# Performance work log

Hardware: AMD Instinct MI355X
Metric: run time of the kernel (lower is better)

## Reference

```python
import jax, jax.numpy as jnp
import numpy as np

B, S, N, D, NAMED, NTYPES = 8, 64, 100, 1024, 768, 5

def _ln(x, g, b, eps=1e-5):
    m = x.mean(-1, keepdims=True)
    v = ((x - m) ** 2).mean(-1, keepdims=True)
    return (x - m) * jax.lax.rsqrt(v + eps) * g + b

def _lin(x, W, b=None):
    y = x @ W.T
    return y if b is None else y + b

def setup_inputs():
    key = jax.random.key(0)
    ks = jax.random.split(key, 24)
    p = lambda i, shape, s=0.02: jax.random.normal(ks[i], shape, jnp.float32) * s
    inp = {}
    inp['scene_reps'] = jax.random.normal(ks[0], (B, S, D), jnp.float32)
    u = jax.random.uniform(ks[1], (B, N, S))
    keep = (jax.random.uniform(ks[2], (B, N, S)) < 0.25).astype(jnp.float32)
    inp['incidence_matrix'] = u * keep
    inp['edge_type_ids'] = jax.random.randint(ks[3], (B, S), 0, NTYPES)
    inp['entity_type_ids'] = jax.random.randint(ks[4], (B, N), 0, NTYPES)
    inp['entity_mask'] = jax.random.uniform(ks[5], (B, N)) < 0.9
    inp['entity_name_embs'] = jax.random.normal(ks[6], (B, N, NAMED), jnp.float32)
    inp['type_embed'] = p(7, (NTYPES, D), 1.0)
    inp['name_W'] = p(8, (D, NAMED))
    inp['name_ln_g'] = jnp.ones(D); inp['name_ln_b'] = jnp.zeros(D)
    inp['n2e_W'] = p(9, (D, D)); inp['n2e_b'] = jnp.zeros(D)
    inp['t2e_W'] = p(10, (D, D)); inp['t2e_b'] = jnp.zeros(D)
    inp['edge_ln_g'] = jnp.ones(D); inp['edge_ln_b'] = jnp.zeros(D)
    inp['gate_W1'] = p(11, (D // 4, D)); inp['gate_b1'] = jnp.zeros(D // 4)
    inp['gate_W2'] = p(12, (3, D // 4)); inp['gate_b2'] = jnp.zeros(3)
    inp['ms_W'] = p(13, (D, D)); inp['ms_b'] = jnp.zeros(D)
    inp['ma_W'] = p(14, (D, D)); inp['ma_b'] = jnp.zeros(D)
    inp['mi_W'] = p(15, (D, D)); inp['mi_b'] = jnp.zeros(D)
    inp['role_w'] = p(16, (D,))
    inp['gru_Wih'] = p(17, (3 * D, D)); inp['gru_Whh'] = p(18, (3 * D, D))
    inp['gru_bih'] = jnp.zeros(3 * D); inp['gru_bhh'] = jnp.zeros(3 * D)
    inp['upd_ln_g'] = jnp.ones(D); inp['upd_ln_b'] = jnp.zeros(D)
    inp['eo_W'] = p(19, (D, D)); inp['eo_b'] = jnp.zeros(D)
    inp['eo_ln_g'] = jnp.ones(D); inp['eo_ln_b'] = jnp.zeros(D)
    inp['res_ln_g'] = jnp.ones(D); inp['res_ln_b'] = jnp.zeros(D)
    return inp

def reference(scene_reps, incidence_matrix, edge_type_ids, entity_type_ids, entity_mask, entity_name_embs, type_embed, name_W, name_ln_g, name_ln_b, n2e_W, n2e_b, t2e_W, t2e_b, edge_ln_g, edge_ln_b, gate_W1, gate_b1, gate_W2, gate_b2, ms_W, ms_b, ma_W, ma_b, mi_W, mi_b, role_w, gru_Wih, gru_Whh, gru_bih, gru_bhh, upd_ln_g, upd_ln_b, eo_W, eo_b, eo_ln_g, eo_ln_b, res_ln_g, res_ln_b):
    # edge_type_ids is accepted by the torch module but unused in its forward.
    dt = scene_reps.dtype
    emaskf = entity_mask.astype(dt)  # [B,N]
    h0 = type_embed[entity_type_ids] + _ln(_lin(entity_name_embs, name_W), name_ln_g, name_ln_b)
    h0 = h0 * emaskf[..., None]
    eye = jnp.eye(N, dtype=dt)
    step_ids = jnp.arange(S)

    def step(carry, xs):
        h, ebuf = carry  # h [B,N,D], ebuf [B,S,D] (hyperedge history)
        s, x_s, inc_s = xs  # x_s [B,D], inc_s [B,N]
        roles = inc_s * emaskf
        wsum = jnp.maximum(roles.sum(1, keepdims=True), 1.0)
        mean_ent = jnp.einsum('bn,bnd->bd', roles, h) / wsum
        e_s = _ln(_lin(mean_ent, n2e_W, n2e_b) + _lin(x_s, t2e_W, t2e_b), edge_ln_g, edge_ln_b)
        in_mask = (roles > 0).astype(dt)[..., None]  # [B,N,1]
        msg_scene = _lin(e_s, ms_W, ms_b)[:, None, :]
        # arc stream: attention over past hyperedges with exponential recency decay
        valid = (step_ids < s).astype(dt)
        denom = jnp.maximum(s - 1, 1).astype(dt)
        decay = jnp.exp(-1.0 + step_ids.astype(dt) / denom) * valid  # linspace(-1,0,s)
        arc = incidence_matrix * roles[:, :, None] * decay[None, None, :]  # [B,N,S]
        arc = arc / jnp.maximum(arc.sum(-1, keepdims=True), 1e-8)
        msg_arc = _lin(jnp.einsum('bns,bsd->bnd', arc, jax.lax.stop_gradient(ebuf)), ma_W, ma_b)
        msg_arc = jnp.where(s > 0, msg_arc, jnp.zeros_like(msg_arc))
        # interaction stream: entity co-occurrence within the scene
        co = roles[:, :, None] * roles[:, None, :] * (1.0 - eye)
        co = co / jnp.maximum(co.sum(-1, keepdims=True), 1e-8)
        msg_int = _lin(jnp.einsum('bnm,bmd->bnd', co, h), mi_W, mi_b)
        gate = jax.nn.softmax(_lin(jax.nn.gelu(_lin(e_s, gate_W1, gate_b1), approximate=False), gate_W2, gate_b2), axis=-1)  # [B,3]
        msg = gate[:, 0, None, None] * msg_scene + gate[:, 1, None, None] * msg_arc + gate[:, 2, None, None] * msg_int
        msg = msg + (roles[..., None] * role_w) * in_mask
        # GRUCell (torch semantics) + LayerNorm, masked update
        gi = _lin(msg, gru_Wih, gru_bih)
        gh = _lin(h, gru_Whh, gru_bhh)
        i_r, i_z, i_n = jnp.split(gi, 3, axis=-1)
        h_r, h_z, h_n = jnp.split(gh, 3, axis=-1)
        r = jax.nn.sigmoid(i_r + h_r)
        z = jax.nn.sigmoid(i_z + h_z)
        n = jnp.tanh(i_n + r * h_n)
        h_new = jnp.clip(_ln((1 - z) * n + z * h, upd_ln_g, upd_ln_b), -50.0, 50.0)
        h = h * (1 - in_mask) + h_new * in_mask
        ebuf = ebuf.at[:, s].set(e_s)
        return (h, ebuf), e_s

    ebuf0 = jnp.zeros((B, S, D), dt)
    (h_fin, _), es = jax.lax.scan(step, (h0, ebuf0), (step_ids, scene_reps.transpose(1, 0, 2), incidence_matrix.transpose(2, 0, 1)))
    H = es.transpose(1, 0, 2)  # [B,S,D]
    H = _ln(H + scene_reps, res_ln_g, res_ln_b)
    H = _ln(jax.nn.gelu(_lin(H, eo_W, eo_b), approximate=False), eo_ln_g, eo_ln_b)
    return (H, h_fin)
```

## Files before the change

kernel.cpp:

```cpp
#include <hip/hip_runtime.h>
#include <math.h>

#define B_   8
#define S_   64
#define N_   100
#define D_   1024
#define ND_  768
#define BN_  800
#define G3_  3072
#define G6_  6144
#define HC7  7168
#define RSC  0.00390625f

typedef _Float16 f16x8 __attribute__((ext_vector_type(8)));
typedef float f32x4 __attribute__((ext_vector_type(4)));

#define MFMA16(a,b,c) __builtin_amdgcn_mfma_f32_16x16x32_f16(a, b, c, 0, 0, 0)

static __device__ __forceinline__ float wave_sum(float v) {
    for (int off = 32; off > 0; off >>= 1) v += __shfl_down(v, off, 64);
    return v;
}

static __device__ __forceinline__ float wave_allsum(float v) {
    for (int off = 1; off < 64; off <<= 1) v += __shfl_xor(v, off, 64);
    return v;
}

static __device__ __forceinline__ float block_sum(float v) {
    __shared__ float red_[8];
    float w = wave_sum(v);
    int lane = threadIdx.x & 63, wid = threadIdx.x >> 6;
    __syncthreads();
    if (lane == 0) red_[wid] = w;
    __syncthreads();
    float t = 0.f;
    for (int i = 0; i < 4; ++i) t += red_[i];
    return t;
}

static __device__ __forceinline__ float gelu_f(float x) {
    return 0.5f * x * (1.f + erff(x * 0.70710678118654752f));
}

static __device__ __forceinline__ unsigned short f2h(float x) {
    union { _Float16 h; unsigned short u; } c; c.h = (_Float16)x; return c.u;
}

__global__ __launch_bounds__(256) void k_f2h(
    const float* __restrict__ src, unsigned short* __restrict__ dst,
    int rows, int cols, int ldd)
{
    size_t n = (size_t)rows * cols;
    size_t i = ((size_t)blockIdx.x * 256 + threadIdx.x) * 4;
    if (i >= n) return;
    int r = (int)(i / cols);
    int c = (int)(i - (size_t)r * cols);
    float4 v = *(const float4*)(src + i);
    ushort4 o; o.x = f2h(v.x); o.y = f2h(v.y); o.z = f2h(v.z); o.w = f2h(v.w);
    *(ushort4*)(dst + (size_t)r * ldd + c) = o;
}

__global__ __launch_bounds__(256) void k_f2hT(
    const float* __restrict__ src, unsigned short* __restrict__ dst,
    int R, int C, int ldd, int rowoff)
{
    __shared__ _Float16 T[32][33];
    int tr = threadIdx.x >> 3, tc4 = (threadIdx.x & 7) * 4;
    int r0 = blockIdx.y * 32, c0 = blockIdx.x * 32;
    float4 v = *(const float4*)(src + (size_t)(r0 + tr) * C + c0 + tc4);
    T[tc4][tr] = (_Float16)v.x; T[tc4+1][tr] = (_Float16)v.y;
    T[tc4+2][tr] = (_Float16)v.z; T[tc4+3][tr] = (_Float16)v.w;
    __syncthreads();
    union { _Float16 h; unsigned short u; } cv;
    ushort4 o;
    cv.h = T[tr][tc4];   o.x = cv.u;
    cv.h = T[tr][tc4+1]; o.y = cv.u;
    cv.h = T[tr][tc4+2]; o.z = cv.u;
    cv.h = T[tr][tc4+3]; o.w = cv.u;
    *(ushort4*)(dst + (size_t)(rowoff + c0 + tr) * ldd + r0 + tc4) = o;
}

__global__ __launch_bounds__(256) void k_mfma16_nt(
    const unsigned short* __restrict__ A16, const unsigned short* __restrict__ W16,
    const float* __restrict__ bias, float* __restrict__ C,
    unsigned short* __restrict__ C16, float oscale,
    int M, int Nc, int K)
{
    int m0 = blockIdx.y * 64; if (m0 >= M) return;
    int n0 = blockIdx.x * 128;
    __shared__ _Float16 sA[64][72];
    __shared__ _Float16 sB[128][72];
    int tid = threadIdx.x;
    int w = tid >> 6, l = tid & 63;
    int l15 = l & 15, q = l >> 4;
    int wn = w * 32;
    int arow = tid >> 3, achk = (tid & 7) * 8;
    f32x4 acc[4][2] = {};
    for (int k0 = 0; k0 < K; k0 += 64) {
        for (int ri = 0; ri < 64; ri += 32) {
            int gm = m0 + arow + ri;
            uint4 v = make_uint4(0u, 0u, 0u, 0u);
            if (gm < M) v = *(const uint4*)(A16 + (size_t)gm * K + k0 + achk);
            *(uint4*)(&sA[arow + ri][achk]) = v;
        }
        for (int i = 0; i < 4; ++i) {
            int r = arow + 32 * i;
            *(uint4*)(&sB[r][achk]) = *(const uint4*)(W16 + (size_t)(n0 + r) * K + k0 + achk);
        }
        __syncthreads();
#pragma unroll
        for (int ks = 0; ks < 64; ks += 32) {
            f16x8 b0 = *(const f16x8*)(&sB[wn + l15][ks + q*8]);
            f16x8 b1 = *(const f16x8*)(&sB[wn + 16 + l15][ks + q*8]);
#pragma unroll
            for (int mi = 0; mi < 4; ++mi) {
                f16x8 a = *(const f16x8*)(&sA[mi*16 + l15][ks + q*8]);
                acc[mi][0] = MFMA16(a, b0, acc[mi][0]);
                acc[mi][1] = MFMA16(a, b1, acc[mi][1]);
            }
        }
        __syncthreads();
    }
    for (int mi = 0; mi < 4; ++mi)
        for (int nj = 0; nj < 2; ++nj)
            for (int r = 0; r < 4; ++r) {
                int gm = m0 + mi*16 + q*4 + r;
                int cl = wn + nj*16 + l15;
                if (gm < M) {
                    size_t off = (size_t)gm * Nc + n0 + cl;
                    float v = acc[mi][nj][r];
                    if (C16) C16[off] = f2h(v * oscale);
                    else C[off] = v + (bias ? bias[n0 + cl] : 0.f);
                }
            }
}

__global__ __launch_bounds__(256) void k_h0(
    const float* __restrict__ P, const int* __restrict__ etype,
    const int* __restrict__ emask, const float* __restrict__ temb,
    const float* __restrict__ g, const float* __restrict__ bt,
    float* __restrict__ h, unsigned short* __restrict__ h16)
{
    int bn = blockIdx.x, tid = threadIdx.x;
    int t = etype[bn], mk = emask[bn];
    float x[4]; float lsum = 0.f;
    for (int k = 0; k < 4; ++k) { x[k] = P[(size_t)bn*D_ + tid + 256*k]; lsum += x[k]; }
    float mean = block_sum(lsum) * (1.f / D_);
    float lv = 0.f;
    for (int k = 0; k < 4; ++k) { float d = x[k] - mean; lv += d * d; }
    float inv = rsqrtf(block_sum(lv) * (1.f / D_) + 1e-5f);
    for (int k = 0; k < 4; ++k) {
        int d = tid + 256*k;
        float y = (x[k] - mean) * inv * g[d] + bt[d];
        float hv = mk ? (temb[(size_t)t*D_ + d] + y) : 0.f;
        h[(size_t)bn*D_ + d] = hv;
        h16[(size_t)bn*D_ + d] = f2h(hv);
    }
}

__global__ __launch_bounds__(256) void k_hcat0(
    const unsigned short* __restrict__ h16, const unsigned short* __restrict__ n2e16,
    const unsigned short* __restrict__ Wmi16, const unsigned short* __restrict__ Whh16,
    float* __restrict__ Hcat)
{
    int m0 = blockIdx.y * 32;
    int n0 = blockIdx.x * 64;
    const unsigned short* Bp; int ldb; int nl;
    if (n0 < 1024)      { Bp = n2e16;        ldb = D_;  nl = n0; }
    else if (n0 < 4096) { Bp = Wmi16 + 2048; ldb = G3_; nl = n0 - 1024; }
    else                { Bp = Whh16;        ldb = D_;  nl = n0 - 4096; }
    __shared__ _Float16 sA[32][72];
    __shared__ _Float16 sB[64][72];
    int tid = threadIdx.x;
    int w = tid >> 6, l = tid & 63;
    int l15 = l & 15, q = l >> 4;
    int wm = (w & 1) * 16, wn = (w >> 1) * 32;
    int arow = tid >> 3, achk = (tid & 7) * 8;
    int gmA = m0 + arow;
    f32x4 acc[2] = {};
    for (int k0 = 0; k0 < D_; k0 += 64) {
        *(uint4*)(&sA[arow][achk]) = *(const uint4*)(h16 + (size_t)gmA*D_ + k0 + achk);
        *(uint4*)(&sB[arow][achk])      = *(const uint4*)(Bp + (size_t)(nl + arow)*ldb + k0 + achk);
        *(uint4*)(&sB[arow + 32][achk]) = *(const uint4*)(Bp + (size_t)(nl + arow + 32)*ldb + k0 + achk);
        __syncthreads();
#pragma unroll
        for (int ks = 0; ks < 64; ks += 32) {
            f16x8 a  = *(const f16x8*)(&sA[wm + l15][ks + q*8]);
            f16x8 b0 = *(const f16x8*)(&sB[wn + l15][ks + q*8]);
            f16x8 b1 = *(const f16x8*)(&sB[wn + 16 + l15][ks + q*8]);
            acc[0] = MFMA16(a, b0, acc[0]);
            acc[1] = MFMA16(a, b1, acc[1]);
        }
        __syncthreads();
    }
    for (int j = 0; j < 2; ++j)
        for (int r = 0; r < 4; ++r) {
            int row = wm + q*4 + r;
            Hcat[(size_t)(m0 + row)*HC7 + n0 + wn + j*16 + l15] = acc[j][r];
        }
}

__global__ __launch_bounds__(256) void k_front(
    const float* __restrict__ inc, const int* __restrict__ emask,
    const float* __restrict__ Esmi, float* __restrict__ arcsum,
    int* __restrict__ cntp, int* __restrict__ lst, float* __restrict__ rro,
    float* __restrict__ scl,
    const int* __restrict__ prevcnt, const int* __restrict__ prevlist,
    const unsigned short* __restrict__ h16, const unsigned short* __restrict__ n2e16,
    const unsigned short* __restrict__ Wmi16, const unsigned short* __restrict__ Whh16,
    float* __restrict__ Hcat, float* __restrict__ gatepre,
    float* __restrict__ esumP, float* __restrict__ TmiP, float* __restrict__ wsumP,
    int s)
{
    int tid = threadIdx.x, bid = blockIdx.x;
    if (bid == 0 && tid < 32) gatepre[tid] = 0.f;
    if (bid < BN_) {
        int m = bid;
        int b = m / N_;
        float r = emask[m] ? inc[(size_t)m*S_ + s] : 0.f;
        if (r <= 0.f) return;
        __shared__ int sidx, nwa;
        __shared__ float wav[S_]; __shared__ int wai[S_];
        if (tid == 0) { sidx = atomicAdd(cntp, 1); nwa = 0; }
        __syncthreads();
        int idx = sidx;
        float denomA = fmaxf((float)(s - 1), 1.f);
        float wa = 0.f;
        if (tid < s) {
            float iv = inc[(size_t)m*S_ + tid];
            if (iv > 0.f) {
                wa = iv * r * expf(-1.f + (float)tid / denomA);
                int p = atomicAdd(&nwa, 1);
                wav[p] = wa; wai[p] = tid;
            }
        }
        float dA = block_sum(wa);
        float rm = 0.f;
        if (tid < N_) rm = emask[b*N_ + tid] ? inc[((size_t)b*N_ + tid)*S_ + s] : 0.f;
        float wsum = block_sum(rm);
        __syncthreads();
        int na = nwa;
        float sclA = 1.f / fmaxf(dA, 1e-8f);
        if (tid == 0) {
            lst[idx] = m; rro[idx] = r;
            scl[idx] = r / fmaxf(r * (wsum - r), 1e-8f);
            wsumP[b] = wsum;
        }
        float rprev = (s > 0) ? inc[(size_t)m*S_ + (s-1)] : 0.f;
        if (rprev <= 0.f) {
            const float4* hp = (const float4*)(Hcat + (size_t)m*HC7);
#pragma unroll
            for (int j2 = 0; j2 < 4; ++j2) {
                float4 hv = hp[tid + 256*j2];
                int c = (tid + 256*j2) * 4;
                float* dst = (c < 1024) ? (esumP + (size_t)b*D_ + c)
                                        : (TmiP + (size_t)b*G3_ + (c - 1024));
                atomicAdd(dst + 0, r*hv.x); atomicAdd(dst + 1, r*hv.y);
                atomicAdd(dst + 2, r*hv.z); atomicAdd(dst + 3, r*hv.w);
            }
        }
        float a12[12];
#pragma unroll
        for (int k = 0; k < 12; ++k) a12[k] = 0.f;
        for (int j = 0; j < na; ++j) {
            float wj = wav[j];
            const float* ep = Esmi + ((size_t)b*S_ + wai[j])*G3_;
#pragma unroll
            for (int k = 0; k < 12; ++k) a12[k] += wj * ep[tid + 256*k];
        }
        float* ao = arcsum + (size_t)idx*G3_;
#pragma unroll
        for (int k = 0; k < 12; ++k) ao[tid + 256*k] = a12[k] * sclA;
    } else {
        int pM = *prevcnt;
        int t = bid - BN_;
        int nt = t % 112, mt = t / 112;
        int m0 = mt * 64;
        if (m0 >= pM) return;
        int n0 = nt * 64;
        const unsigned short* Bp; int ldb; int nl;
        if (n0 < 1024)      { Bp = n2e16;        ldb = D_;  nl = n0; }
        else if (n0 < 4096) { Bp = Wmi16 + 2048; ldb = G3_; nl = n0 - 1024; }
        else                { Bp = Whh16;        ldb = D_;  nl = n0 - 4096; }
        __shared__ _Float16 sA[64][72];
        __shared__ _Float16 sB[64][72];
        __shared__ int slist[64];
        __shared__ float srn[64];
        __shared__ int sbb[64];
        if (tid < 64) {
            int gm = m0 + tid;
            int m = (gm < pM) ? prevlist[gm] : 0;
            slist[tid] = m;
            float rn = 0.f;
            if (gm < pM) rn = emask[m] ? inc[(size_t)m*S_ + s] : 0.f;
            srn[tid] = rn;
            sbb[tid] = m / N_;
        }
        __syncthreads();
        int w = tid >> 6, l = tid & 63;
        int l15 = l & 15, q = l >> 4;
        int wm = (w & 1) * 32, wn = (w >> 1) * 32;
        int arow = tid >> 3, achk = (tid & 7) * 8;
        f32x4 acc[2][2] = {};
        for (int k0 = 0; k0 < D_; k0 += 64) {
            for (int ri = 0; ri < 64; ri += 32) {
                int row = arow + ri, gm = m0 + row;
                uint4 v = make_uint4(0u,0u,0u,0u);
                if (gm < pM) v = *(const uint4*)(h16 + (size_t)slist[row]*D_ + k0 + achk);
                *(uint4*)(&sA[row][achk]) = v;
            }
            *(uint4*)(&sB[arow][achk])      = *(const uint4*)(Bp + (size_t)(nl + arow)*ldb + k0 + achk);
            *(uint4*)(&sB[arow + 32][achk]) = *(const uint4*)(Bp + (size_t)(nl + arow + 32)*ldb + k0 + achk);
            __syncthreads();
#pragma unroll
            for (int ks = 0; ks < 64; ks += 32) {
                f16x8 a0 = *(const f16x8*)(&sA[wm + l15][ks + q*8]);
                f16x8 a1 = *(const f16x8*)(&sA[wm + 16 + l15][ks + q*8]);
                f16x8 b0 = *(const f16x8*)(&sB[wn + l15][ks + q*8]);
                f16x8 b1 = *(const f16x8*)(&sB[wn + 16 + l15][ks + q*8]);
                acc[0][0] = MFMA16(a0, b0, acc[0][0]);
                acc[0][1] = MFMA16(a0, b1, acc[0][1]);
                acc[1][0] = MFMA16(a1, b0, acc[1][0]);
                acc[1][1] = MFMA16(a1, b1, acc[1][1]);
            }
            __syncthreads();
        }
        for (int mi = 0; mi < 2; ++mi)
            for (int nj = 0; nj < 2; ++nj)
                for (int r = 0; r < 4; ++r) {
                    int row = wm + mi*16 + q*4 + r;
                    int gm = m0 + row;
                    if (gm < pM) {
                        float v = acc[mi][nj][r];
                        int c = n0 + wn + nj*16 + l15;
                        Hcat[(size_t)slist[row]*HC7 + c] = v;
                        float rn = srn[row];
                        if (rn > 0.f && c < 4096) {
                            float* dst = (c < 1024)
                                ? (esumP + (size_t)sbb[row]*D_ + c)
                                : (TmiP + (size_t)sbb[row]*G3_ + (c - 1024));
                            atomicAdd(dst, rn * v);
                        }
                    }
                }
    }
}

__global__ __launch_bounds__(256) void k_mid(
    const float* __restrict__ esumP, const float* __restrict__ wsumP,
    float* __restrict__ esumZ, float* __restrict__ TmiZ, float* __restrict__ wsumZ,
    const float* __restrict__ n2eb, const float* __restrict__ pre_t2e,
    const float* __restrict__ elng, const float* __restrict__ elnb,
    const float* __restrict__ gW1, const float* __restrict__ gb1,
    const float* __restrict__ gW2, const unsigned short* __restrict__ Wmi16,
    float* __restrict__ esbuf, float* __restrict__ gatepre,
    float* __restrict__ Emi, float* __restrict__ Esmi,
    int* __restrict__ ctrl, int par, int s)
{
    int bid = blockIdx.x, tid = threadIdx.x;
    if (bid < 32) {
        __shared__ float se[D_];
        int b = bid >> 2, seg = bid & 3;
        if (bid == 0 && tid == 0) ctrl[1 - par] = 0;
        esumZ[(size_t)b*D_ + seg*256 + tid] = 0.f;
#pragma unroll
        for (int j = 0; j < 3; ++j) TmiZ[(size_t)b*G3_ + seg*768 + j*256 + tid] = 0.f;
        if (seg == 0 && tid == 0) wsumZ[b] = 0.f;
        float invw = 1.f / fmaxf(wsumP[b], 1.f);
        float4 ev = ((const float4*)(esumP + (size_t)b*D_))[tid];
        float4 nb = ((const float4*)n2eb)[tid];
        float4 pt = ((const float4*)(pre_t2e + ((size_t)b*S_ + s)*D_))[tid];
        float x[4] = { ev.x*invw + nb.x + pt.x, ev.y*invw + nb.y + pt.y,
                       ev.z*invw + nb.z + pt.z, ev.w*invw + nb.w + pt.w };
        float mean = block_sum(x[0]+x[1]+x[2]+x[3]) * (1.f / D_);
        float lv = 0.f;
#pragma unroll
        for (int k = 0; k < 4; ++k) { float d = x[k] - mean; lv += d * d; }
        float inv = rsqrtf(block_sum(lv) * (1.f / D_) + 1e-5f);
        float4 lg = ((const float4*)elng)[tid];
        float4 lb = ((const float4*)elnb)[tid];
        float y0 = (x[0]-mean)*inv*lg.x + lb.x;
        float y1 = (x[1]-mean)*inv*lg.y + lb.y;
        float y2 = (x[2]-mean)*inv*lg.z + lb.z;
        float y3 = (x[3]-mean)*inv*lg.w + lb.w;
        int d4 = tid * 4;
        se[d4] = y0; se[d4+1] = y1; se[d4+2] = y2; se[d4+3] = y3;
        if (seg == 0)
            ((float4*)(esbuf + ((size_t)b*S_ + s)*D_))[tid] = make_float4(y0,y1,y2,y3);
        __syncthreads();
        if (tid < 64) {
            int u = seg * 64 + tid;
            float acc = gb1[u];
            const float* w1 = gW1 + (size_t)u * D_;
            for (int j = 0; j < D_; j += 4) {
                float4 w = *(const float4*)(w1 + j);
                acc += w.x*se[j] + w.y*se[j+1] + w.z*se[j+2] + w.w*se[j+3];
            }
            float hg = gelu_f(acc);
            for (int c = 0; c < 3; ++c) {
                float p = wave_sum(gW2[c*256 + u] * hg);
                if (tid == 0) atomicAdd(gatepre + b*4 + c, p);
            }
        }
    } else {
        __shared__ float se32[8][1028];
        int w = tid >> 6, lane = tid & 63;
        for (int bb = 0; bb < 2; ++bb) {
            int b = w*2 + bb;
            float invw = 1.f / fmaxf(wsumP[b], 1.f);
            int d0 = lane * 16;
            const float4* ep = (const float4*)(esumP + (size_t)b*D_ + d0);
            const float4* np = (const float4*)(n2eb + d0);
            const float4* pp = (const float4*)(pre_t2e + ((size_t)b*S_ + s)*D_ + d0);
            float x[16]; float sm = 0.f;
#pragma unroll
            for (int j = 0; j < 4; ++j) {
                float4 e = ep[j], n = np[j], p = pp[j];
                x[j*4+0] = e.x*invw + n.x + p.x;
                x[j*4+1] = e.y*invw + n.y + p.y;
                x[j*4+2] = e.z*invw + n.z + p.z;
                x[j*4+3] = e.w*invw + n.w + p.w;
                sm += x[j*4+0] + x[j*4+1] + x[j*4+2] + x[j*4+3];
            }
            float mean = wave_allsum(sm) * (1.f / D_);
            float lv = 0.f;
#pragma unroll
            for (int j = 0; j < 16; ++j) { float d = x[j] - mean; lv += d * d; }
            float inv = rsqrtf(wave_allsum(lv) * (1.f / D_) + 1e-5f);
            const float4* lgp = (const float4*)(elng + d0);
            const float4* lbp = (const float4*)(elnb + d0);
#pragma unroll
            for (int j = 0; j < 4; ++j) {
                float4 lg = lgp[j], lb = lbp[j];
                se32[b][d0 + j*4 + 0] = (x[j*4+0]-mean)*inv*lg.x + lb.x;
                se32[b][d0 + j*4 + 1] = (x[j*4+1]-mean)*inv*lg.y + lb.y;
                se32[b][d0 + j*4 + 2] = (x[j*4+2]-mean)*inv*lg.z + lb.z;
                se32[b][d0 + j*4 + 3] = (x[j*4+3]-mean)*inv*lg.w + lb.w;
            }
        }
        __syncthreads();
        int c0 = (bid - 32) * 32;
        int colg = tid >> 5, t31 = tid & 31;
        int cb = c0 + colg * 4;
        float accA[4][8] = {};
        float accB[4][8] = {};
#pragma unroll
        for (int i = 0; i < 8; ++i) {
            int kh = t31*4 + i*128;
            float wf[4][4];
#pragma unroll
            for (int c = 0; c < 4; ++c) {
                union { uint2 u; _Float16 h[4]; } cv;
                cv.u = *(const uint2*)(Wmi16 + (size_t)(cb + c)*G3_ + kh);
                wf[c][0] = (float)cv.h[0]; wf[c][1] = (float)cv.h[1];
                wf[c][2] = (float)cv.h[2]; wf[c][3] = (float)cv.h[3];
            }
#pragma unroll
            for (int b = 0; b < 8; ++b) {
                float4 sv = *(const float4*)(&se32[b][kh]);
#pragma unroll
                for (int c = 0; c < 4; ++c)
                    accA[c][b] += wf[c][0]*sv.x + wf[c][1]*sv.y
                                + wf[c][2]*sv.z + wf[c][3]*sv.w;
            }
        }
#pragma unroll
        for (int i = 0; i < 8; ++i) {
            int kh = t31*4 + i*128;
            float wf[4][4];
#pragma unroll
            for (int c = 0; c < 4; ++c) {
                union { uint2 u; _Float16 h[4]; } cv;
                cv.u = *(const uint2*)(Wmi16 + (size_t)(cb + c)*G3_ + 1024 + kh);
                wf[c][0] = (float)cv.h[0]; wf[c][1] = (float)cv.h[1];
                wf[c][2] = (float)cv.h[2]; wf[c][3] = (float)cv.h[3];
            }
#pragma unroll
            for (int b = 0; b < 8; ++b) {
                float4 sv = *(const float4*)(&se32[b][kh]);
#pragma unroll
                for (int c = 0; c < 4; ++c)
                    accB[c][b] += wf[c][0]*sv.x + wf[c][1]*sv.y
                                + wf[c][2]*sv.z + wf[c][3]*sv.w;
            }
        }
#pragma unroll
        for (int off = 16; off >= 1; off >>= 1) {
#pragma unroll
            for (int c = 0; c < 4; ++c)
#pragma unroll
                for (int b = 0; b < 8; ++b) {
                    accA[c][b] += __shfl_down(accA[c][b], off, 32);
                    accB[c][b] += __shfl_down(accB[c][b], off, 32);
                }
        }
        if (t31 == 0) {
#pragma unroll
            for (int c = 0; c < 4; ++c) {
                int col = cb + c;
#pragma unroll
                for (int b = 0; b < 8; ++b) {
                    Emi[(size_t)b*G3_ + col] = accA[c][b];
                    Esmi[((size_t)b*S_ + s)*G3_ + col] = accB[c][b];
                }
            }
        }
    }
}

__global__ __launch_bounds__(256) void k_fin(
    const int* __restrict__ lst, const int* __restrict__ cntp,
    const float* __restrict__ rro, const float* __restrict__ scl,
    const float* __restrict__ gatepre, const float* __restrict__ gb2,
    const float* __restrict__ Hcat, const float* __restrict__ Emi,
    const float* __restrict__ arcsum, const float* __restrict__ Tmi,
    const float* __restrict__ gBm, const float* __restrict__ bih,
    const float* __restrict__ bhh,
    const float* __restrict__ ulng, const float* __restrict__ ulnb,
    float* __restrict__ h, unsigned short* __restrict__ h16, int s)
{
    int row = blockIdx.x;
    if (row >= *cntp) return;
    int bn = lst[row];
    int b = bn / N_;
    int tid = threadIdx.x;
    float t0 = gatepre[b*4+0] + gb2[0];
    float t1 = gatepre[b*4+1] + gb2[1];
    float t2 = gatepre[b*4+2] + gb2[2];
    float mx = fmaxf(t0, fmaxf(t1, t2));
    float e0 = expf(t0-mx), e1 = expf(t1-mx), e2 = expf(t2-mx);
    float si = 1.f / (e0 + e1 + e2);
    float g0 = e0*si, g1 = (s > 0) ? e1*si : 0.f, g2 = e2*si;
    float rv = rro[row];
    float sI = scl[row];
    const float* Hrow = Hcat + (size_t)bn * HC7;
    const float* em = Emi + (size_t)b * G3_;
    const float* as = arcsum + (size_t)row * G3_;
    const float* tm = Tmi + (size_t)b * G3_;
    float u[4]; float lsum = 0.f;
    for (int k = 0; k < 4; ++k) {
        int d = tid + 256*k;
        float ip[3];
#pragma unroll
        for (int c = 0; c < 3; ++c) {
            int dd = c*D_ + d;
            float gint = tm[dd] - rv * Hrow[1024 + dd];
            ip[c] = RSC * (g0*em[dd] + g1*as[dd] + g2*sI*gint)
                  + g0*gBm[dd] + g1*gBm[G3_ + dd] + g2*gBm[2*G3_ + dd]
                  + rv*gBm[3*G3_ + dd] + bih[dd];
        }
        float hr = Hrow[4096 + d]        + bhh[d];
        float hz = Hrow[4096 + D_ + d]   + bhh[D_ + d];
        float hn = Hrow[4096 + 2*D_ + d] + bhh[2*D_ + d];
        float hv = h[(size_t)bn*D_ + d];
        float r = 1.f / (1.f + expf(-(ip[0] + hr)));
        float z = 1.f / (1.f + expf(-(ip[1] + hz)));
        float nn = tanhf(ip[2] + r * hn);
        u[k] = (1.f - z) * nn + z * hv;
        lsum += u[k];
    }
    float mean = block_sum(lsum) * (1.f / D_);
    float lv = 0.f;
    for (int k = 0; k < 4; ++k) { float d = u[k] - mean; lv += d * d; }
    float inv = rsqrtf(block_sum(lv) * (1.f / D_) + 1e-5f);
    for (int k = 0; k < 4; ++k) {
        int d = tid + 256*k;
        float y = (u[k] - mean) * inv * ulng[d] + ulnb[d];
        y = fminf(fmaxf(y, -50.f), 50.f);
        h[(size_t)bn*D_ + d] = y;
        h16[(size_t)bn*D_ + d] = f2h(y);
    }
}

__global__ __launch_bounds__(256) void k_resln(
    float* __restrict__ buf, const float* __restrict__ scene,
    const float* __restrict__ g, const float* __restrict__ bt,
    unsigned short* __restrict__ H16)
{
    size_t row = blockIdx.x;
    int tid = threadIdx.x;
    float x[4]; float lsum = 0.f;
    for (int k = 0; k < 4; ++k) {
        int d = tid + 256*k;
        x[k] = buf[row*D_ + d] + scene[row*D_ + d];
        lsum += x[k];
    }
    float mean = block_sum(lsum) * (1.f / D_);
    float lv = 0.f;
    for (int k = 0; k < 4; ++k) { float d = x[k] - mean; lv += d * d; }
    float inv = rsqrtf(block_sum(lv) * (1.f / D_) + 1e-5f);
    for (int k = 0; k < 4; ++k) {
        int d = tid + 256*k;
        float y = (x[k] - mean) * inv * g[d] + bt[d];
        buf[row*D_ + d] = y;
        H16[row*D_ + d] = f2h(y);
    }
}

__global__ __launch_bounds__(256) void k_final(
    const float* __restrict__ G, const float* __restrict__ g, const float* __restrict__ bt,
    float* __restrict__ outH, const float* __restrict__ h, float* __restrict__ outh)
{
    int tid = threadIdx.x;
    if (blockIdx.x < B_*S_) {
        size_t row = blockIdx.x;
        float x[4]; float lsum = 0.f;
        for (int k = 0; k < 4; ++k) {
            x[k] = gelu_f(G[row*D_ + tid + 256*k]);
            lsum += x[k];
        }
        float mean = block_sum(lsum) * (1.f / D_);
        float lv = 0.f;
        for (int k = 0; k < 4; ++k) { float d = x[k] - mean; lv += d * d; }
        float inv = rsqrtf(block_sum(lv) * (1.f / D_) + 1e-5f);
        for (int k = 0; k < 4; ++k) {
            int d = tid + 256*k;
            outH[row*D_ + d] = (x[k] - mean) * inv * g[d] + bt[d];
        }
    } else {
        size_t bn = blockIdx.x - B_*S_;
        for (int d = tid; d < D_; d += 256)
            outh[bn*D_ + d] = h[bn*D_ + d];
    }
}

extern "C" void kernel_launch(void* const* d_in, const int* in_sizes, int n_in,
                              void* d_out, int out_size, void* d_ws, size_t ws_size,
                              hipStream_t stream)
{
    const float* scene = (const float*)d_in[0];
    const float* inc   = (const float*)d_in[1];
    const int*   etype = (const int*)d_in[3];
    const int*   emask = (const int*)d_in[4];
    const float* nemb  = (const float*)d_in[5];
    const float* temb  = (const float*)d_in[6];
    const float* nameW = (const float*)d_in[7];
    const float* nlg   = (const float*)d_in[8];
    const float* nlb   = (const float*)d_in[9];
    const float* n2eW  = (const float*)d_in[10];
    const float* n2eb  = (const float*)d_in[11];
    const float* t2eW  = (const float*)d_in[12];
    const float* t2eb  = (const float*)d_in[13];
    const float* elng  = (const float*)d_in[14];
    const float* elnb  = (const float*)d_in[15];
    const float* gW1   = (const float*)d_in[16];
    const float* gb1   = (const float*)d_in[17];
    const float* gW2   = (const float*)d_in[18];
    const float* gb2   = (const float*)d_in[19];
    const float* msW   = (const float*)d_in[20];
    const float* msB   = (const float*)d_in[21];
    const float* maW   = (const float*)d_in[22];
    const float* maB   = (const float*)d_in[23];
    const float* miW   = (const float*)d_in[24];
    const float* miB   = (const float*)d_in[25];
    const float* rolew = (const float*)d_in[26];
    const float* Wih   = (const float*)d_in[27];
    const float* Whh   = (const float*)d_in[28];
    const float* bih   = (const float*)d_in[29];
    const float* bhh   = (const float*)d_in[30];
    const float* ulng  = (const float*)d_in[31];
    const float* ulnb  = (const float*)d_in[32];
    const float* eoW   = (const float*)d_in[33];
    const float* eoB   = (const float*)d_in[34];
    const float* eolng = (const float*)d_in[35];
    const float* eolnb = (const float*)d_in[36];
    const float* rlng  = (const float*)d_in[37];
    const float* rlnb  = (const float*)d_in[38];

    float* outH = (float*)d_out;
    float* outh = outH + (size_t)B_*S_*D_;

    float* W = (float*)d_ws;
    size_t o = 0;
    int*   ctrl     = (int*)(W + o); o += 64;
    float* esum2    = W + o; o += 2*(size_t)B_*D_;
    float* Tmi2     = W + o; o += 2*(size_t)B_*G3_;
    float* wsum2    = W + o; o += 16;
    float* gatepre  = W + o; o += 32;
    float* rowrole  = W + o; o += 2*BN_;
    float* sclbuf   = W + o; o += BN_;
    int*   list     = (int*)(W + o); o += 2*BN_;
    float* hbuf     = W + o; o += (size_t)BN_*D_;
    float* Hcat     = W + o; o += (size_t)BN_*HC7;
    float* pre_t2e  = W + o; o += (size_t)B_*S_*D_;
    float* gBm      = W + o; o += 4*G3_;
    float* Emi      = W + o; o += (size_t)B_*G3_;
    float* Esmi     = W + o; o += (size_t)B_*S_*G3_;
    float* arcsum   = W + o; o += (size_t)BN_*G3_;
    float* tmp      = W + o; o += (size_t)BN_*D_;
    unsigned short* U = (unsigned short*)(W + o);
    size_t uo = 0;
    unsigned short* h16    = U + uo; uo += (size_t)BN_*D_;
    unsigned short* H16    = U + uo; uo += (size_t)B_*S_*D_;
    unsigned short* Wih16  = U + uo; uo += (size_t)G3_*D_;
    unsigned short* Whh16  = U + uo; uo += (size_t)G3_*D_;
    unsigned short* n2e16  = U + uo; uo += (size_t)D_*D_;
    unsigned short* eoW16  = U + uo; uo += (size_t)D_*D_;
    unsigned short* nW16   = U + uo; uo += (size_t)D_*ND_;
    unsigned short* nE16   = U + uo; uo += (size_t)BN_*ND_;
    unsigned short* t2e16  = U + uo; uo += (size_t)D_*D_;
    unsigned short* sc16   = U + uo; uo += (size_t)B_*S_*D_;
    unsigned short* WcatT16= U + uo; uo += (size_t)G3_*D_;
    unsigned short* Wmi16  = U + uo; uo += (size_t)G3_*G3_;
    unsigned short* bias4  = U + uo; uo += 4*D_;

    hipMemsetAsync(ctrl, 0,
        (64 + 2*(size_t)B_*D_ + 2*(size_t)B_*G3_ + 16) * sizeof(float), stream);

    #define CVT(src, dst, r, c, ld) \
        k_f2h<<<(((size_t)(r)*(c)/4 + 255)/256), 256, 0, stream>>>(src, dst, r, c, ld)
    CVT(Wih,   Wih16, G3_, D_,  D_);
    CVT(Whh,   Whh16, G3_, D_,  D_);
    CVT(n2eW,  n2e16, D_,  D_,  D_);
    CVT(nameW, nW16,  D_,  ND_, ND_);
    CVT(nemb,  nE16,  BN_, ND_, ND_);
    CVT(eoW,   eoW16, D_,  D_,  D_);
    CVT(t2eW,  t2e16, D_,  D_,  D_);
    CVT(scene, sc16,  B_*S_, D_, D_);
    CVT(msB,   bias4 + 0,    1, D_, D_);
    CVT(maB,   bias4 + D_,   1, D_, D_);
    CVT(miB,   bias4 + 2*D_, 1, D_, D_);
    CVT(rolew, bias4 + 3*D_, 1, D_, D_);
    #undef CVT
    k_f2hT<<<dim3(32,32), 256, 0, stream>>>(msW, WcatT16, D_, D_, D_, 0);
    k_f2hT<<<dim3(32,32), 256, 0, stream>>>(maW, WcatT16, D_, D_, D_, D_);
    k_f2hT<<<dim3(32,32), 256, 0, stream>>>(miW, WcatT16, D_, D_, D_, 2*D_);

    k_mfma16_nt<<<dim3(G3_/128, G3_/64), 256, 0, stream>>>(
        Wih16, WcatT16, nullptr, nullptr, Wmi16, 256.f, G3_, G3_, D_);
    k_mfma16_nt<<<dim3(G3_/128, 1), 256, 0, stream>>>(
        bias4, Wih16, nullptr, gBm, nullptr, 1.f, 4, G3_, D_);
    k_mfma16_nt<<<dim3(D_/128, (B_*S_+63)/64), 256, 0, stream>>>(
        sc16, t2e16, t2eb, pre_t2e, nullptr, 1.f, B_*S_, D_, D_);
    k_mfma16_nt<<<dim3(D_/128, (BN_+63)/64), 256, 0, stream>>>(
        nE16, nW16, nullptr, tmp, nullptr, 1.f, BN_, D_, ND_);
    k_h0<<<BN_, 256, 0, stream>>>(tmp, etype, emask, temb, nlg, nlb, hbuf, h16);
    k_hcat0<<<dim3(112, 25), 256, 0, stream>>>(h16, n2e16, Wmi16, Whh16, Hcat);

    for (int s = 0; s < S_; ++s) {
        int par = s & 1;
        int*   cntp = ctrl + par;
        int*   pcnt = ctrl + (1 - par);
        int*   lst  = list + par * BN_;
        int*   plst = list + (1 - par) * BN_;
        float* rro  = rowrole + par * BN_;
        float* esumP = esum2 + (size_t)par * B_*D_;
        float* esumZ = esum2 + (size_t)(1 - par) * B_*D_;
        float* TmiP  = Tmi2 + (size_t)par * B_*G3_;
        float* TmiZ  = Tmi2 + (size_t)(1 - par) * B_*G3_;
        float* wsumP = wsum2 + par * 8;
        float* wsumZ = wsum2 + (1 - par) * 8;
        k_front<<<BN_ + 112*13, 256, 0, stream>>>(inc, emask, Esmi, arcsum,
            cntp, lst, rro, sclbuf, pcnt, plst, h16, n2e16, Wmi16, Whh16,
            Hcat, gatepre, esumP, TmiP, wsumP, s);
        k_mid<<<128, 256, 0, stream>>>(esumP, wsumP, esumZ, TmiZ, wsumZ,
            n2eb, pre_t2e, elng, elnb, gW1, gb1, gW2, Wmi16,
            outH, gatepre, Emi, Esmi, ctrl, par, s);
        k_fin<<<BN_, 256, 0, stream>>>(lst, cntp, rro, sclbuf, gatepre, gb2,
            Hcat, Emi, arcsum, TmiP, gBm, bih, bhh, ulng, ulnb, hbuf, h16, s);
    }

    k_resln<<<B_*S_, 256, 0, stream>>>(outH, scene, rlng, rlnb, H16);
    k_mfma16_nt<<<dim3(D_/128, (B_*S_+63)/64), 256, 0, stream>>>(
        H16, eoW16, eoB, tmp, nullptr, 1.f, B_*S_, D_, D_);
    k_final<<<B_*S_ + BN_, 256, 0, stream>>>(tmp, eolng, eolnb, outH, hbuf, outh);
}
```

Baseline: 4.203 ms.

## Enlarge gathered GEMM M-tile to 256 rows in k_front and vectorize arc sums

The gathered-row GEMM inside k_front now has each block cover up to 256 active rows (four 64-row subtiles) against one 64-column weight tile, reusing the B tile across subtiles. The grid shrinks from 112*13 to 448 GEMM blocks, and the shared memory is unioned with the arc-sum path's scratch. The arc-weighted Esmi accumulation also switches to float4 loads and stores. The larger tile cuts redundant weight loads but leaves fewer blocks to run in parallel, and it raises register use (64 accumulators per thread) and LDS use (about 46KB per block).

```diff
diff --git a/kernel.cpp b/kernel.cpp
--- a/kernel.cpp
+++ b/kernel.cpp
@@ -8,8 +8,8 @@
 #define ND_  768
 #define BN_  800
 #define G3_  3072
-#define G6_  6144
 #define HC7  7168
+#define GMT  448
 #define RSC  0.00390625f
 
 typedef _Float16 f16x8 __attribute__((ext_vector_type(8)));
@@ -201,6 +201,12 @@
         }
 }
 
+union SMF {
+    struct { _Float16 A[256][72]; _Float16 Bm[64][72];
+             int slist[256]; float srn[256]; int sbb[256]; } g;
+    struct { float wav[S_]; int wai[S_]; } r;
+};
+
 __global__ __launch_bounds__(256) void k_front(
     const float* __restrict__ inc, const int* __restrict__ emask,
     const float* __restrict__ Esmi, float* __restrict__ arcsum,
@@ -213,6 +219,8 @@
     float* __restrict__ esumP, float* __restrict__ TmiP, float* __restrict__ wsumP,
     int s)
 {
+    __shared__ SMF sm;
+    __shared__ int sidx, nwa;
     int tid = threadIdx.x, bid = blockIdx.x;
     if (bid == 0 && tid < 32) gatepre[tid] = 0.f;
     if (bid < BN_) {
@@ -220,8 +228,6 @@
         int b = m / N_;
         float r = emask[m] ? inc[(size_t)m*S_ + s] : 0.f;
         if (r <= 0.f) return;
-        __shared__ int sidx, nwa;
-        __shared__ float wav[S_]; __shared__ int wai[S_];
         if (tid == 0) { sidx = atomicAdd(cntp, 1); nwa = 0; }
         __syncthreads();
         int idx = sidx;
@@ -232,7 +238,7 @@
             if (iv > 0.f) {
                 wa = iv * r * expf(-1.f + (float)tid / denomA);
                 int p = atomicAdd(&nwa, 1);
-                wav[p] = wa; wai[p] = tid;
+                sm.r.wav[p] = wa; sm.r.wai[p] = tid;
             }
         }
         float dA = block_sum(wa);
@@ -260,90 +266,104 @@
                 atomicAdd(dst + 2, r*hv.z); atomicAdd(dst + 3, r*hv.w);
             }
         }
-        float a12[12];
-#pragma unroll
-        for (int k = 0; k < 12; ++k) a12[k] = 0.f;
+        float4 a4[3];
+#pragma unroll
+        for (int k = 0; k < 3; ++k) a4[k] = make_float4(0.f,0.f,0.f,0.f);
         for (int j = 0; j < na; ++j) {
-            float wj = wav[j];
-            const float* ep = Esmi + ((size_t)b*S_ + wai[j])*G3_;
-#pragma unroll
-            for (int k = 0; k < 12; ++k) a12[k] += wj * ep[tid + 256*k];
-        }
-        float* ao = arcsum + (size_t)idx*G3_;
-#pragma unroll
-        for (int k = 0; k < 12; ++k) ao[tid + 256*k] = a12[k] * sclA;
+            float wj = sm.r.wav[j];
+            const float4* ep = (const float4*)(Esmi + ((size_t)b*S_ + sm.r.wai[j])*G3_);
+#pragma unroll
+            for (int k = 0; k < 3; ++k) {
+                float4 e = ep[tid + 256*k];
+                a4[k].x += wj*e.x; a4[k].y += wj*e.y;
+                a4[k].z += wj*e.z; a4[k].w += wj*e.w;
+            }
+        }
+        float4* ao = (float4*)(arcsum + (size_t)idx*G3_);
+#pragma unroll
+        for (int k = 0; k < 3; ++k) {
+            float4 v = make_float4(a4[k].x*sclA, a4[k].y*sclA,
+                                   a4[k].z*sclA, a4[k].w*sclA);
+            ao[tid + 256*k] = v;
+        }
     } else {
         int pM = *prevcnt;
         int t = bid - BN_;
-        int nt = t % 112, mt = t / 112;
-        int m0 = mt * 64;
+        int nt = t % 112, mg = t / 112;
+        int m0 = mg * 256;
         if (m0 >= pM) return;
         int n0 = nt * 64;
         const unsigned short* Bp; int ldb; int nl;
         if (n0 < 1024)      { Bp = n2e16;        ldb = D_;  nl = n0; }
         else if (n0 < 4096) { Bp = Wmi16 + 2048; ldb = G3_; nl = n0 - 1024; }
         else                { Bp = Whh16;        ldb = D_;  nl = n0 - 4096; }
-        __shared__ _Float16 sA[64][72];
-        __shared__ _Float16 sB[64][72];
-        __shared__ int slist[64];
-        __shared__ float srn[64];
-        __shared__ int sbb[64];
-        if (tid < 64) {
+        {
             int gm = m0 + tid;
             int m = (gm < pM) ? prevlist[gm] : 0;
-            slist[tid] = m;
+            sm.g.slist[tid] = m;
             float rn = 0.f;
             if (gm < pM) rn = emask[m] ? inc[(size_t)m*S_ + s] : 0.f;
-            srn[tid] = rn;
-            sbb[tid] = m / N_;
+            sm.g.srn[tid] = rn;
+            sm.g.sbb[tid] = m / N_;
         }
         __syncthreads();
         int w = tid >> 6, l = tid & 63;
         int l15 = l & 15, q = l >> 4;
         int wm = (w & 1) * 32, wn = (w >> 1) * 32;
         int arow = tid >> 3, achk = (tid & 7) * 8;
-        f32x4 acc[2][2] = {};
+        int nmt = (pM - m0 + 63) >> 6; if (nmt > 4) nmt = 4;
+        int nrow = nmt * 64;
+        f32x4 acc[4][2][2] = {};
         for (int k0 = 0; k0 < D_; k0 += 64) {
-            for (int ri = 0; ri < 64; ri += 32) {
+            for (int ri = 0; ri < nrow; ri += 32) {
                 int row = arow + ri, gm = m0 + row;
                 uint4 v = make_uint4(0u,0u,0u,0u);
-                if (gm < pM) v = *(const uint4*)(h16 + (size_t)slist[row]*D_ + k0 + achk);
-                *(uint4*)(&sA[row][achk]) = v;
-            }
-            *(uint4*)(&sB[arow][achk])      = *(const uint4*)(Bp + (size_t)(nl + arow)*ldb + k0 + achk);
-            *(uint4*)(&sB[arow + 32][achk]) = *(const uint4*)(Bp + (size_t)(nl + arow + 32)*ldb + k0 + achk);
+                if (gm < pM) v = *(const uint4*)(h16 + (size_t)sm.g.slist[row]*D_ + k0 + achk);
+                *(uint4*)(&sm.g.A[row][achk]) = v;
+            }
+            *(uint4*)(&sm.g.Bm[arow][achk])      = *(const uint4*)(Bp + (size_t)(nl + arow)*ldb + k0 + achk);
+            *(uint4*)(&sm.g.Bm[arow + 32][achk]) = *(const uint4*)(Bp + (size_t)(nl + arow + 32)*ldb + k0 + achk);
             __syncthreads();
 #pragma unroll
             for (int ks = 0; ks < 64; ks += 32) {
-                f16x8 a0 = *(const f16x8*)(&sA[wm + l15][ks + q*8]);
-                f16x8 a1 = *(const f16x8*)(&sA[wm + 16 + l15][ks + q*8]);
-                f16x8 b0 = *(const f16x8*)(&sB[wn + l15][ks + q*8]);
-                f16x8 b1 = *(const f16x8*)(&sB[wn + 16 + l15][ks + q*8]);
-                acc[0][0] = MFMA16(a0, b0, acc[0][0]);
-                acc[0][1] = MFMA16(a0, b1, acc[0][1]);
-                acc[1][0] = MFMA16(a1, b0, acc[1][0]);
-                acc[1][1] = MFMA16(a1, b1, acc[1][1]);
+                f16x8 b0 = *(const f16x8*)(&sm.g.Bm[wn + l15][ks + q*8]);
+                f16x8 b1 = *(const f16x8*)(&sm.g.Bm[wn + 16 + l15][ks + q*8]);
+#pragma unroll
+                for (int mt = 0; mt < 4; ++mt) {
+                    if (mt < nmt) {
+                        f16x8 a0 = *(const f16x8*)(&sm.g.A[mt*64 + wm + l15][ks + q*8]);
+                        f16x8 a1 = *(const f16x8*)(&sm.g.A[mt*64 + wm + 16 + l15][ks + q*8]);
+                        acc[mt][0][0] = MFMA16(a0, b0, acc[mt][0][0]);
+                        acc[mt][0][1] = MFMA16(a0, b1, acc[mt][0][1]);
+                        acc[mt][1][0] = MFMA16(a1, b0, acc[mt][1][0]);
+                        acc[mt][1][1] = MFMA16(a1, b1, acc[mt][1][1]);
+                    }
+                }
             }
             __syncthreads();
         }
-        for (int mi = 0; mi < 2; ++mi)
-            for (int nj = 0; nj < 2; ++nj)
-                for (int r = 0; r < 4; ++r) {
-                    int row = wm + mi*16 + q*4 + r;
-                    int gm = m0 + row;
-                    if (gm < pM) {
-                        float v = acc[mi][nj][r];
-                        int c = n0 + wn + nj*16 + l15;
-                        Hcat[(size_t)slist[row]*HC7 + c] = v;
-                        float rn = srn[row];
-                        if (rn > 0.f && c < 4096) {
-                            float* dst = (c < 1024)
-                                ? (esumP + (size_t)sbb[row]*D_ + c)
-                                : (TmiP + (size_t)sbb[row]*G3_ + (c - 1024));
-                            atomicAdd(dst, rn * v);
+#pragma unroll
+        for (int mt = 0; mt < 4; ++mt) {
+            if (mt >= nmt) continue;
+            for (int mi = 0; mi < 2; ++mi)
+                for (int nj = 0; nj < 2; ++nj)
+                    for (int r4 = 0; r4 < 4; ++r4) {
+                        int row = mt*64 + wm + mi*16 + q*4 + r4;
+                        int gm = m0 + row;
+                        if (gm < pM) {
+                            float v = acc[mt][mi][nj][r4];
+                            int c = n0 + wn + nj*16 + l15;
+                            Hcat[(size_t)sm.g.slist[row]*HC7 + c] = v;
+                            float rn = sm.g.srn[row];
+                            if (rn > 0.f && c < 4096) {
+                                float* dst = (c < 1024)
+                                    ? (esumP + (size_t)sm.g.sbb[row]*D_ + c)
+                                    : (TmiP + (size_t)sm.g.sbb[row]*G3_ + (c - 1024));
+                                atomicAdd(dst, rn * v);
+                            }
                         }
                     }
-                }
+        }
     }
 }
 
@@ -413,7 +433,7 @@
             const float4* ep = (const float4*)(esumP + (size_t)b*D_ + d0);
             const float4* np = (const float4*)(n2eb + d0);
             const float4* pp = (const float4*)(pre_t2e + ((size_t)b*S_ + s)*D_ + d0);
-            float x[16]; float sm = 0.f;
+            float x[16]; float smv = 0.f;
 #pragma unroll
             for (int j = 0; j < 4; ++j) {
                 float4 e = ep[j], n = np[j], p = pp[j];
@@ -421,9 +441,9 @@
                 x[j*4+1] = e.y*invw + n.y + p.y;
                 x[j*4+2] = e.z*invw + n.z + p.z;
                 x[j*4+3] = e.w*invw + n.w + p.w;
-                sm += x[j*4+0] + x[j*4+1] + x[j*4+2] + x[j*4+3];
-            }
-            float mean = wave_allsum(sm) * (1.f / D_);
+                smv += x[j*4+0] + x[j*4+1] + x[j*4+2] + x[j*4+3];
+            }
+            float mean = wave_allsum(smv) * (1.f / D_);
             float lv = 0.f;
 #pragma unroll
             for (int j = 0; j < 16; ++j) { float d = x[j] - mean; lv += d * d; }
@@ -751,7 +771,7 @@
         float* TmiZ  = Tmi2 + (size_t)(1 - par) * B_*G3_;
         float* wsumP = wsum2 + par * 8;
         float* wsumZ = wsum2 + (1 - par) * 8;
-        k_front<<<BN_ + 112*13, 256, 0, stream>>>(inc, emask, Esmi, arcsum,
+        k_front<<<BN_ + GMT, 256, 0, stream>>>(inc, emask, Esmi, arcsum,
             cntp, lst, rro, sclbuf, pcnt, plst, h16, n2e16, Wmi16, Whh16,
             Hcat, gatepre, esumP, TmiP, wsumP, s);
         k_mid<<<128, 256, 0, stream>>>(esumP, wsumP, esumZ, TmiZ, wsumZ,
```

Result: slower. 7.570 ms (+80.1%).
